# Kernel tuning notes

Hardware: AMD Instinct MI355X
Metric: run time of the kernel (lower is better)

The kernel has to match this reference:

```python
import jax, jax.numpy as jnp
import numpy as np
import math

B, S, D, H, CD = 8, 1024, 1024, 16, 512
HD = D // H
LN_EPS = 1e-5


def _layernorm(x, g, b):
    mu = jnp.mean(x, axis=-1, keepdims=True)
    var = jnp.var(x, axis=-1, keepdims=True)
    return (x - mu) / jnp.sqrt(var + LN_EPS) * g + b


def _modlin(x, code, wc_w, wc_b, ln_g, ln_b, W, b):
    # transformed_code: LayerNorm(Linear(code)) -> [D]
    tc = _layernorm(code @ wc_w.T + wc_b, ln_g, ln_b)
    return (tc * x) @ W.T + b


def setup_inputs() -> dict:
    key = jax.random.key(0)
    ks = jax.random.split(key, 16)
    inp = {
        'query': jax.random.normal(ks[0], (B, S, D), jnp.float32),
        'key': jax.random.normal(ks[1], (B, S, D), jnp.float32),
        'value': jax.random.normal(ks[2], (B, S, D), jnp.float32),
        'compability_u': jax.random.uniform(ks[3], (B, S), jnp.float32),
        'code': jax.random.normal(ks[4], (CD,), jnp.float32),
        'W': jax.random.normal(ks[5], (D, D), jnp.float32) * 0.02,
        'b': jnp.zeros((D,), jnp.float32),
    }
    for i, p in enumerate(['q', 'k', 'v', 'o']):
        inp[p + '_wc_w'] = jax.random.normal(ks[6 + i], (D, CD), jnp.float32) * 0.02
        inp[p + '_wc_b'] = jnp.zeros((D,), jnp.float32)
        inp[p + '_ln_g'] = jnp.ones((D,), jnp.float32)
        inp[p + '_ln_b'] = jnp.zeros((D,), jnp.float32)
    return inp


def reference(query, key, value, compability_u, code, W, b,
              q_wc_w, q_wc_b, q_ln_g, q_ln_b,
              k_wc_w, k_wc_b, k_ln_g, k_ln_b,
              v_wc_w, v_wc_b, v_ln_g, v_ln_b,
              o_wc_w, o_wc_b, o_ln_g, o_ln_b):
    Q = _modlin(query, code, q_wc_w, q_wc_b, q_ln_g, q_ln_b, W, b)
    K = _modlin(key, code, k_wc_w, k_wc_b, k_ln_g, k_ln_b, W, b)
    V = _modlin(value, code, v_wc_w, v_wc_b, v_ln_g, v_ln_b, W, b)
    # [B,S,D] -> [B,H,S,HD]
    Q = Q.reshape(B, S, H, HD).transpose(0, 2, 1, 3)
    K = K.reshape(B, S, H, HD).transpose(0, 2, 1, 3)
    V = V.reshape(B, S, H, HD).transpose(0, 2, 1, 3)
    energy = jnp.einsum('bhid,bhjd->bhij', Q, K) / math.sqrt(HD)
    attention = jax.nn.softmax(energy, axis=-1)
    # c_u_i[b,h,i,j] = u[b,i]; c_u_j[b,h,i,j] = u[b,j]
    attention = compability_u[:, None, :, None] * compability_u[:, None, None, :] * attention
    attention = attention / (1e-6 + attention)
    x = jnp.einsum('bhij,bhjd->bhid', attention, V)  # dropout p=0 (eval)
    x = x.transpose(0, 2, 1, 3).reshape(B, S, D)
    x = _modlin(x, code, o_wc_w, o_wc_b, o_ln_g, o_ln_b, W, b)
    return x, attention
```

## Files before the change

kernel.cpp:

```cpp
#include <hip/hip_runtime.h>
#include <hip/hip_bf16.h>
#include <stdint.h>

typedef __bf16 bf16_t;
typedef __attribute__((ext_vector_type(8))) __bf16 bf16x8;
typedef __attribute__((ext_vector_type(4))) float f32x4;

#define B_  8
#define S_  1024
#define D_  1024
#define H_  16
#define HD_ 64
#define CD_ 512

typedef __attribute__((address_space(1))) const unsigned int* gas_ptr;
typedef __attribute__((address_space(3))) unsigned int* las_ptr;

__device__ __forceinline__ void gl2lds16(const void* g, void* l) {
    __builtin_amdgcn_global_load_lds((gas_ptr)(unsigned long long)g,
                                     (las_ptr)(unsigned long long)l, 16, 0, 0);
}

__device__ __forceinline__ float clamp30(float x) {
    return fminf(fmaxf(x, -30.f), 30.f);
}

__global__ void detect_kernel(const unsigned int* Wbits, int* flag) {
    __shared__ int cnt[64];
    int c = 0;
    for (int i = threadIdx.x; i < 512; i += 64) {
        unsigned int w = Wbits[i];
        unsigned int e = (w >> 7) & 0xFFu;
        c += (e >= 0x66u && e <= 0x7Fu) ? 1 : 0;
    }
    cnt[threadIdx.x] = c;
    __syncthreads();
    if (threadIdx.x == 0) {
        int t = 0;
        for (int i = 0; i < 64; ++i) t += cnt[i];
        *flag = (t >= 280) ? 0 : 1;
    }
}

#define CANON_TOTAL 28333568u
struct CanonArgs {
    const void* src[23];
    bf16_t* dst[23];
    unsigned int off[24];
    const int* flag;
};

__global__ __launch_bounds__(256) void canon_kernel(CanonArgs a) {
    const bool f32 = (*a.flag != 0);
    const unsigned int e = ((unsigned int)blockIdx.x * 256u + threadIdx.x) * 8u;
    if (e >= CANON_TOTAL) return;
    int t = 0;
    while (e >= a.off[t + 1]) ++t;
    const unsigned int le = e - a.off[t];
    bf16_t* d = a.dst[t] + le;
    if (f32) {
        const float* s = (const float*)a.src[t] + le;
        bf16x8 o;
#pragma unroll
        for (int j = 0; j < 8; ++j) o[j] = (bf16_t)s[j];
        *(bf16x8*)d = o;
    } else {
        *(uint4*)d = *(const uint4*)((const bf16_t*)a.src[t] + le);
    }
}

struct TCArgs {
    const bf16_t* code;
    const bf16_t* bglob;
    const bf16_t* wcw[4];
    const bf16_t* wcb[4];
    const bf16_t* lng[4];
    const bf16_t* lnb[4];
    float* tc;
    float* biasArr;
};

__global__ __launch_bounds__(256) void tc_kernel(TCArgs a) {
    const int p = blockIdx.x;
    const int tid = threadIdx.x;
    __shared__ float codeS[CD_];
    __shared__ float red[256];
    __shared__ float bcast[2];
    for (int c = tid; c < CD_; c += 256) codeS[c] = (float)a.code[c];
    __syncthreads();
    float y[4];
    const bf16_t* wcw = a.wcw[p];
    for (int j = 0; j < 4; ++j) {
        const int d = tid + j * 256;
        float acc = (float)a.wcb[p][d];
        const bf16x8* row = (const bf16x8*)(wcw + (size_t)d * CD_);
        for (int c8 = 0; c8 < CD_ / 8; ++c8) {
            bf16x8 v = row[c8];
#pragma unroll
            for (int t = 0; t < 8; ++t) acc += codeS[c8 * 8 + t] * (float)v[t];
        }
        y[j] = acc;
    }
    float s = y[0] + y[1] + y[2] + y[3];
    red[tid] = s;
    __syncthreads();
    for (int off = 128; off > 0; off >>= 1) {
        if (tid < off) red[tid] += red[tid + off];
        __syncthreads();
    }
    if (tid == 0) bcast[0] = red[0] * (1.0f / (float)D_);
    __syncthreads();
    const float mu = bcast[0];
    float sq = 0.f;
    for (int j = 0; j < 4; ++j) { float t = y[j] - mu; sq += t * t; }
    red[tid] = sq;
    __syncthreads();
    for (int off = 128; off > 0; off >>= 1) {
        if (tid < off) red[tid] += red[tid + off];
        __syncthreads();
    }
    if (tid == 0) bcast[1] = red[0] * (1.0f / (float)D_);
    __syncthreads();
    const float rstd = rsqrtf(bcast[1] + 1e-5f);
    const float scale = (p == 0) ? 0.125f : 1.0f;
    for (int j = 0; j < 4; ++j) {
        const int d = tid + j * 256;
        float tcv = ((y[j] - mu) * rstd * (float)a.lng[p][d] + (float)a.lnb[p][d]) * scale;
        a.tc[p * D_ + d] = tcv;
        a.biasArr[p * D_ + d] = (float)a.bglob[d] * scale;
    }
}

__global__ __launch_bounds__(256) void wscale_kernel(const bf16_t* __restrict__ W,
                                                     const float* __restrict__ tc,
                                                     bf16_t* __restrict__ Wp) {
    const size_t idx = (size_t)blockIdx.x * 256 + threadIdx.x;
    const size_t e = idx * 8;
    const int p = (int)(e >> 20);
    const size_t rem = e & 1048575;
    const int k = (int)(rem & 1023);
    bf16x8 w = *(const bf16x8*)(W + rem);
    const float* t = tc + p * 1024 + k;
    bf16x8 o;
#pragma unroll
    for (int j = 0; j < 8; ++j) o[j] = (bf16_t)((float)w[j] * t[j]);
    *(bf16x8*)(Wp + e) = o;
}

__global__ __launch_bounds__(256) void gemm_bt(const bf16_t* __restrict__ A0,
                                               const bf16_t* __restrict__ A1,
                                               const bf16_t* __restrict__ A2,
                                               const bf16_t* __restrict__ WpAll,
                                               const float* __restrict__ biasAll,
                                               void* Cbase, int pBase, int dualOut,
                                               const int* flagp) {
    constexpr int Kd = 1024, Nd = 1024;
    __shared__ __align__(16) bf16_t As[128 * 32];
    __shared__ __align__(16) bf16_t Bs[128 * 32];
    const int tid = threadIdx.x;
    const int pl = blockIdx.y >> 6;
    const int p = pBase + pl;
    const bf16_t* A = (pl == 0) ? A0 : ((pl == 1) ? A1 : A2);
    const bf16_t* Bw = WpAll + (size_t)p * 1024 * 1024;
    const size_t cOff = (size_t)pl * 8388608;
    const int rowBase = (blockIdx.y & 63) * 128;
    const int colBase = blockIdx.x * 128;
    const int lane = tid & 63;
    const int wv = tid >> 6;
    const int wm = wv >> 1, wn = wv & 1;
    const int qd = lane >> 4, cl = lane & 15;

    f32x4 acc[4][4];
#pragma unroll
    for (int tn = 0; tn < 4; ++tn) {
        float bv = biasAll[p * 1024 + colBase + wn * 64 + tn * 16 + cl];
#pragma unroll
        for (int tm = 0; tm < 4; ++tm) acc[tm][tn] = (f32x4){bv, bv, bv, bv};
    }

    for (int kb = 0; kb < Kd; kb += 32) {
#pragma unroll
        for (int cc = 0; cc < 2; ++cc) {
            const int s = tid + cc * 256;
            const int rw = s >> 2;
            const int co = (s & 3) * 8;
            gl2lds16(A + (size_t)(rowBase + rw) * Kd + kb + co,
                     (char*)As + wv * 1024 + cc * 4096);
            gl2lds16(Bw + (size_t)(colBase + rw) * Kd + kb + co,
                     (char*)Bs + wv * 1024 + cc * 4096);
        }
        __syncthreads();
        bf16x8 aF[4], bF[4];
#pragma unroll
        for (int tm = 0; tm < 4; ++tm)
            aF[tm] = *(const bf16x8*)&As[(wm * 64 + tm * 16 + cl) * 32 + qd * 8];
#pragma unroll
        for (int tn = 0; tn < 4; ++tn)
            bF[tn] = *(const bf16x8*)&Bs[(wn * 64 + tn * 16 + cl) * 32 + qd * 8];
#pragma unroll
        for (int tm = 0; tm < 4; ++tm)
#pragma unroll
            for (int tn = 0; tn < 4; ++tn)
                acc[tm][tn] = __builtin_amdgcn_mfma_f32_16x16x32_bf16(aF[tm], bF[tn],
                                                                      acc[tm][tn], 0, 0, 0);
        __syncthreads();
    }
    const bool f32o = (dualOut != 0) && (*flagp != 0);
    if (f32o) {
        float* Cf = (float*)Cbase + cOff;
#pragma unroll
        for (int tm = 0; tm < 4; ++tm)
#pragma unroll
            for (int tn = 0; tn < 4; ++tn)
#pragma unroll
                for (int r = 0; r < 4; ++r) {
                    const int row = rowBase + wm * 64 + tm * 16 + qd * 4 + r;
                    const int col = colBase + wn * 64 + tn * 16 + cl;
                    Cf[(size_t)row * Nd + col] = acc[tm][tn][r];
                }
    } else {
        bf16_t* Cb = (bf16_t*)Cbase + cOff;
#pragma unroll
        for (int tm = 0; tm < 4; ++tm)
#pragma unroll
            for (int tn = 0; tn < 4; ++tn)
#pragma unroll
                for (int r = 0; r < 4; ++r) {
                    const int row = rowBase + wm * 64 + tm * 16 + qd * 4 + r;
                    const int col = colBase + wn * 64 + tn * 16 + cl;
                    Cb[(size_t)row * Nd + col] = (bf16_t)acc[tm][tn][r];
                }
    }
}

__global__ __launch_bounds__(256) void vtrans(const bf16_t* __restrict__ V,
                                              bf16_t* __restrict__ Vt) {
    __shared__ __align__(16) bf16_t T[64][72];
    const int bh = blockIdx.y, b = bh >> 4, h = bh & 15;
    const int s0 = blockIdx.x * 64;
    const int tid = threadIdx.x;
    const int rr = tid >> 3, cc8 = (tid & 7) * 8;
#pragma unroll
    for (int it = 0; it < 2; ++it) {
        const int sr = rr + it * 32;
        bf16x8 v = *(const bf16x8*)&V[((size_t)(b * S_ + s0 + sr)) * D_ + h * HD_ + cc8];
#pragma unroll
        for (int j = 0; j < 8; ++j) T[cc8 + j][sr] = v[j];
    }
    __syncthreads();
#pragma unroll
    for (int it = 0; it < 2; ++it) {
        const int dr = rr + it * 32;
        bf16x8 o;
#pragma unroll
        for (int j = 0; j < 8; ++j) o[j] = T[dr][cc8 + j];
        *(bf16x8*)&Vt[((size_t)bh * 64 + dr) * S_ + s0 + cc8] = o;
    }
}

__global__ __launch_bounds__(256) void attn_fused(const bf16_t* __restrict__ Q,
                                                  const bf16_t* __restrict__ Kmat,
                                                  const bf16_t* __restrict__ Vt,
                                                  const bf16_t* __restrict__ u,
                                                  void* outBase,
                                                  bf16_t* __restrict__ Xatt,
                                                  const int* flagp) {
    __shared__ __align__(16) bf16_t Ks[32 * 64];
    __shared__ __align__(16) bf16_t Vs[64 * 32];
    __shared__ __align__(16) bf16_t P[4][512];
    __shared__ __align__(16) bf16_t uS[S_];
    const int bh = blockIdx.y, b = bh >> 4, h = bh & 15;
    const int tid = threadIdx.x, lane = tid & 63, wv = tid >> 6;
    const int i0 = blockIdx.x * 64 + wv * 16;
    const int qd = lane >> 4, cl = lane & 15;
    const bool f32o = (*flagp != 0);
    float* attF = (float*)outBase + 8388608;
    bf16_t* attB = (bf16_t*)outBase + 8388608;

    for (int t = tid; t < S_ / 8; t += 256)
        *(bf16x8*)&uS[t * 8] = *(const bf16x8*)&u[b * S_ + t * 8];

    const bf16_t* Qb = Q + ((size_t)(b * S_ + i0 + cl)) * D_ + h * HD_ + qd * 8;
    bf16x8 aQ0 = *(const bf16x8*)Qb;
    bf16x8 aQ1 = *(const bf16x8*)(Qb + 32);

    const int srow_k = tid >> 3;
    const int scol_k = ((tid & 7) * 16) ^ ((srow_k & 7) << 4);
    const bf16_t* Ksrc = Kmat + ((size_t)(b * S_) + srow_k) * D_ + h * HD_ + (scol_k >> 1);
    const int srow_v = tid >> 2;
    const int scol_v = ((tid & 3) * 16) ^ ((srow_v & 3) << 4);
    const bf16_t* Vsrc = Vt + ((size_t)bh * 64 + srow_v) * S_ + (scol_v >> 1);

    f32x4 l = {0.f, 0.f, 0.f, 0.f};
    for (int jb = 0; jb < S_; jb += 32) {
        gl2lds16(Ksrc + (size_t)jb * D_, (char*)Ks + tid * 16);
        __syncthreads();
#pragma unroll
        for (int js = 0; js < 2; ++js) {
            const int rj = js * 16 + cl;
            const char* kr = (const char*)Ks + rj * 128;
            const int sw = (rj & 7) << 4;
            bf16x8 k0 = *(const bf16x8*)(kr + ((qd * 16) ^ sw));
            bf16x8 k1 = *(const bf16x8*)(kr + ((64 + qd * 16) ^ sw));
            f32x4 e = {0.f, 0.f, 0.f, 0.f};
            e = __builtin_amdgcn_mfma_f32_16x16x32_bf16(aQ0, k0, e, 0, 0, 0);
            e = __builtin_amdgcn_mfma_f32_16x16x32_bf16(aQ1, k1, e, 0, 0, 0);
            l.x += __expf(clamp30(e.x));
            l.y += __expf(clamp30(e.y));
            l.z += __expf(clamp30(e.z));
            l.w += __expf(clamp30(e.w));
        }
        __syncthreads();
    }
    for (int m = 1; m < 16; m <<= 1) {
        l.x += __shfl_xor(l.x, m);
        l.y += __shfl_xor(l.y, m);
        l.z += __shfl_xor(l.z, m);
        l.w += __shfl_xor(l.w, m);
    }
    float ui[4], el[4];
    const float lv[4] = {l.x, l.y, l.z, l.w};
#pragma unroll
    for (int r = 0; r < 4; ++r) {
        ui[r] = (float)uS[i0 + qd * 4 + r];
        el[r] = fmaxf(1e-6f * lv[r], 0.f);
    }

    f32x4 accPV[4];
#pragma unroll
    for (int dt = 0; dt < 4; ++dt) accPV[dt] = (f32x4){0.f, 0.f, 0.f, 0.f};
    bf16_t* Pw = P[wv];

    for (int jb = 0; jb < S_; jb += 32) {
        gl2lds16(Ksrc + (size_t)jb * D_, (char*)Ks + tid * 16);
        gl2lds16(Vsrc + jb, (char*)Vs + tid * 16);
        __syncthreads();
#pragma unroll
        for (int js = 0; js < 2; ++js) {
            const int rj = js * 16 + cl;
            const char* kr = (const char*)Ks + rj * 128;
            const int sw = (rj & 7) << 4;
            bf16x8 k0 = *(const bf16x8*)(kr + ((qd * 16) ^ sw));
            bf16x8 k1 = *(const bf16x8*)(kr + ((64 + qd * 16) ^ sw));
            f32x4 e = {0.f, 0.f, 0.f, 0.f};
            e = __builtin_amdgcn_mfma_f32_16x16x32_bf16(aQ0, k0, e, 0, 0, 0);
            e = __builtin_amdgcn_mfma_f32_16x16x32_bf16(aQ1, k1, e, 0, 0, 0);
            const int j0 = jb + js * 16;
            const float uj = (float)uS[j0 + cl];
#pragma unroll
            for (int r = 0; r < 4; ++r) {
                float t = __expf(clamp30(e[r]));
                float num = ui[r] * uj * t;
                float att = num * __builtin_amdgcn_rcpf(el[r] + num);
                const size_t aidx = ((size_t)bh * S_ + i0 + qd * 4 + r) * S_ + j0 + cl;
                if (f32o) attF[aidx] = att;
                else attB[aidx] = (bf16_t)att;
                Pw[(qd * 4 + r) * 32 + js * 16 + cl] = (bf16_t)att;
            }
        }
        bf16x8 pA = *(const bf16x8*)&Pw[cl * 32 + qd * 8];
#pragma unroll
        for (int dt = 0; dt < 4; ++dt) {
            const int rd = dt * 16 + cl;
            const char* vr = (const char*)Vs + rd * 64;
            bf16x8 vF = *(const bf16x8*)(vr + ((qd * 16) ^ ((rd & 3) << 4)));
            accPV[dt] = __builtin_amdgcn_mfma_f32_16x16x32_bf16(pA, vF, accPV[dt], 0, 0, 0);
        }
        __syncthreads();
    }
#pragma unroll
    for (int dt = 0; dt < 4; ++dt)
#pragma unroll
        for (int r = 0; r < 4; ++r)
            Xatt[((size_t)(b * S_ + i0 + qd * 4 + r)) * D_ + h * HD_ + dt * 16 + cl] =
                (bf16_t)accPV[dt][r];
}

extern "C" void kernel_launch(void* const* d_in, const int* in_sizes, int n_in,
                              void* d_out, int out_size, void* d_ws, size_t ws_size,
                              hipStream_t stream) {
    float* tc      = (float*)d_ws;
    float* biasArr = tc + 4096;
    bf16_t* Wp     = (bf16_t*)(biasArr + 4096);
    bf16_t* QKV    = Wp + (size_t)4 * 1048576;
    bf16_t* Xatt   = QKV + (size_t)3 * 8388608;
    bf16_t* Vt     = Xatt + 8388608;
    float* lsum    = (float*)(Vt + 8388608);
    bf16_t* smallC = (bf16_t*)(lsum + 131072);
    bf16_t* cu     = smallC;
    bf16_t* ccode  = cu + 8192;
    bf16_t* cb     = ccode + 512;
    bf16_t* cwcb   = cb + 1024;
    bf16_t* clng   = cwcb + 4096;
    bf16_t* clnb   = clng + 4096;
    int* flagp     = (int*)(clnb + 4096);

    char* canonBase = (char*)d_out + 227540992;
    bf16_t* cQ   = (bf16_t*)canonBase;
    bf16_t* cK   = cQ + 8388608;
    bf16_t* cV   = cK + 8388608;
    bf16_t* cW   = cV + 8388608;
    bf16_t* cwcw = cW + 1048576;

    detect_kernel<<<1, 64, 0, stream>>>((const unsigned int*)d_in[5], flagp);

    CanonArgs ca;
    const unsigned int offs[24] = {
        0u, 8388608u, 16777216u, 25165824u, 25174016u, 25174528u, 26223104u, 26224128u,
        26748416u, 26749440u, 26750464u, 26751488u,
        27275776u, 27276800u, 27277824u, 27278848u,
        27803136u, 27804160u, 27805184u, 27806208u,
        28330496u, 28331520u, 28332544u, 28333568u};
    for (int i = 0; i < 24; ++i) ca.off[i] = offs[i];
    ca.flag = flagp;
    ca.src[0] = d_in[0]; ca.dst[0] = cQ;
    ca.src[1] = d_in[1]; ca.dst[1] = cK;
    ca.src[2] = d_in[2]; ca.dst[2] = cV;
    ca.src[3] = d_in[3]; ca.dst[3] = cu;
    ca.src[4] = d_in[4]; ca.dst[4] = ccode;
    ca.src[5] = d_in[5]; ca.dst[5] = cW;
    ca.src[6] = d_in[6]; ca.dst[6] = cb;
    for (int p = 0; p < 4; ++p) {
        ca.src[7 + 4 * p]  = d_in[7 + 4 * p];  ca.dst[7 + 4 * p]  = cwcw + p * 524288;
        ca.src[8 + 4 * p]  = d_in[8 + 4 * p];  ca.dst[8 + 4 * p]  = cwcb + p * 1024;
        ca.src[9 + 4 * p]  = d_in[9 + 4 * p];  ca.dst[9 + 4 * p]  = clng + p * 1024;
        ca.src[10 + 4 * p] = d_in[10 + 4 * p]; ca.dst[10 + 4 * p] = clnb + p * 1024;
    }
    canon_kernel<<<13835, 256, 0, stream>>>(ca);

    TCArgs ta;
    ta.code = ccode;
    ta.bglob = cb;
    for (int p = 0; p < 4; ++p) {
        ta.wcw[p] = cwcw + p * 524288;
        ta.wcb[p] = cwcb + p * 1024;
        ta.lng[p] = clng + p * 1024;
        ta.lnb[p] = clnb + p * 1024;
    }
    ta.tc = tc;
    ta.biasArr = biasArr;
    tc_kernel<<<4, 256, 0, stream>>>(ta);

    wscale_kernel<<<2048, 256, 0, stream>>>(cW, tc, Wp);
    gemm_bt<<<dim3(8, 192), 256, 0, stream>>>(cQ, cK, cV, Wp, biasArr, QKV, 0, 0, flagp);
    vtrans<<<dim3(16, 128), 256, 0, stream>>>(QKV + (size_t)2 * 8388608, Vt);
    attn_fused<<<dim3(16, 128), 256, 0, stream>>>(QKV, QKV + 8388608, Vt, cu, d_out,
                                                  Xatt, flagp);
    gemm_bt<<<dim3(8, 64), 256, 0, stream>>>(Xatt, Xatt, Xatt, Wp, biasArr, d_out, 3, 1,
                                             flagp);
}
```

Before: 1.046 ms.

## Double-buffer K/V tiles in attention, remap block order for XCDs, raise MFMA priority

The attention kernel now double-buffers the K and V LDS tiles, prefetching the next 32-column tile while the current one is computed, and drops one barrier per iteration. Both the GEMM and attention kernels remap block IDs so that consecutive blocks on the same XCD share rows and heads, which should improve L2 reuse. s_setprio brackets around MFMA sections let compute waves take issue priority. The attention kernel uses more LDS, which may lower occupancy. The single remaining barrier per iteration must also cover the write-after-read hazard on the alternate buffer.

Result: faster. 1.006 ms (-3.8%).

```diff
diff --git a/kernel.cpp b/kernel.cpp
--- a/kernel.cpp
+++ b/kernel.cpp
@@ -158,13 +158,16 @@
     __shared__ __align__(16) bf16_t As[128 * 32];
     __shared__ __align__(16) bf16_t Bs[128 * 32];
     const int tid = threadIdx.x;
-    const int pl = blockIdx.y >> 6;
+    const int bid0 = blockIdx.x + 8 * blockIdx.y;
+    const int bids = (bid0 & 7) * gridDim.y + (bid0 >> 3);
+    const int bgx = bids & 7, bgy = bids >> 3;
+    const int pl = bgy >> 6;
     const int p = pBase + pl;
     const bf16_t* A = (pl == 0) ? A0 : ((pl == 1) ? A1 : A2);
     const bf16_t* Bw = WpAll + (size_t)p * 1024 * 1024;
     const size_t cOff = (size_t)pl * 8388608;
-    const int rowBase = (blockIdx.y & 63) * 128;
-    const int colBase = blockIdx.x * 128;
+    const int rowBase = (bgy & 63) * 128;
+    const int colBase = bgx * 128;
     const int lane = tid & 63;
     const int wv = tid >> 6;
     const int wm = wv >> 1, wn = wv & 1;
@@ -197,12 +200,14 @@
 #pragma unroll
         for (int tn = 0; tn < 4; ++tn)
             bF[tn] = *(const bf16x8*)&Bs[(wn * 64 + tn * 16 + cl) * 32 + qd * 8];
+        __builtin_amdgcn_s_setprio(1);
 #pragma unroll
         for (int tm = 0; tm < 4; ++tm)
 #pragma unroll
             for (int tn = 0; tn < 4; ++tn)
                 acc[tm][tn] = __builtin_amdgcn_mfma_f32_16x16x32_bf16(aF[tm], bF[tn],
                                                                       acc[tm][tn], 0, 0, 0);
+        __builtin_amdgcn_s_setprio(0);
         __syncthreads();
     }
     const bool f32o = (dualOut != 0) && (*flagp != 0);
@@ -265,13 +270,16 @@
                                                   void* outBase,
                                                   bf16_t* __restrict__ Xatt,
                                                   const int* flagp) {
-    __shared__ __align__(16) bf16_t Ks[32 * 64];
-    __shared__ __align__(16) bf16_t Vs[64 * 32];
+    __shared__ __align__(16) bf16_t Ks[2][32 * 64];
+    __shared__ __align__(16) bf16_t Vs[2][64 * 32];
     __shared__ __align__(16) bf16_t P[4][512];
     __shared__ __align__(16) bf16_t uS[S_];
-    const int bh = blockIdx.y, b = bh >> 4, h = bh & 15;
+    const int bid0 = blockIdx.x + 16 * blockIdx.y;
+    const int bids = (bid0 & 7) * 256 + (bid0 >> 3);
+    const int bx = bids & 15, bh = bids >> 4;
+    const int b = bh >> 4, h = bh & 15;
     const int tid = threadIdx.x, lane = tid & 63, wv = tid >> 6;
-    const int i0 = blockIdx.x * 64 + wv * 16;
+    const int i0 = bx * 64 + wv * 16;
     const int qd = lane >> 4, cl = lane & 15;
     const bool f32o = (*flagp != 0);
     float* attF = (float*)outBase + 8388608;
@@ -291,20 +299,25 @@
     const int scol_v = ((tid & 3) * 16) ^ ((srow_v & 3) << 4);
     const bf16_t* Vsrc = Vt + ((size_t)bh * 64 + srow_v) * S_ + (scol_v >> 1);
 
+    gl2lds16(Ksrc, (char*)Ks[0] + tid * 16);
+    __syncthreads();
     f32x4 l = {0.f, 0.f, 0.f, 0.f};
     for (int jb = 0; jb < S_; jb += 32) {
-        gl2lds16(Ksrc + (size_t)jb * D_, (char*)Ks + tid * 16);
-        __syncthreads();
+        const int cur = (jb >> 5) & 1;
+        if (jb + 32 < S_)
+            gl2lds16(Ksrc + (size_t)(jb + 32) * D_, (char*)Ks[cur ^ 1] + tid * 16);
 #pragma unroll
         for (int js = 0; js < 2; ++js) {
             const int rj = js * 16 + cl;
-            const char* kr = (const char*)Ks + rj * 128;
+            const char* kr = (const char*)Ks[cur] + rj * 128;
             const int sw = (rj & 7) << 4;
             bf16x8 k0 = *(const bf16x8*)(kr + ((qd * 16) ^ sw));
             bf16x8 k1 = *(const bf16x8*)(kr + ((64 + qd * 16) ^ sw));
             f32x4 e = {0.f, 0.f, 0.f, 0.f};
+            __builtin_amdgcn_s_setprio(1);
             e = __builtin_amdgcn_mfma_f32_16x16x32_bf16(aQ0, k0, e, 0, 0, 0);
             e = __builtin_amdgcn_mfma_f32_16x16x32_bf16(aQ1, k1, e, 0, 0, 0);
+            __builtin_amdgcn_s_setprio(0);
             l.x += __expf(clamp30(e.x));
             l.y += __expf(clamp30(e.y));
             l.z += __expf(clamp30(e.z));
@@ -331,20 +344,27 @@
     for (int dt = 0; dt < 4; ++dt) accPV[dt] = (f32x4){0.f, 0.f, 0.f, 0.f};
     bf16_t* Pw = P[wv];
 
+    gl2lds16(Ksrc, (char*)Ks[0] + tid * 16);
+    gl2lds16(Vsrc, (char*)Vs[0] + tid * 16);
+    __syncthreads();
     for (int jb = 0; jb < S_; jb += 32) {
-        gl2lds16(Ksrc + (size_t)jb * D_, (char*)Ks + tid * 16);
-        gl2lds16(Vsrc + jb, (char*)Vs + tid * 16);
-        __syncthreads();
+        const int cur = (jb >> 5) & 1;
+        if (jb + 32 < S_) {
+            gl2lds16(Ksrc + (size_t)(jb + 32) * D_, (char*)Ks[cur ^ 1] + tid * 16);
+            gl2lds16(Vsrc + (jb + 32), (char*)Vs[cur ^ 1] + tid * 16);
+        }
 #pragma unroll
         for (int js = 0; js < 2; ++js) {
             const int rj = js * 16 + cl;
-            const char* kr = (const char*)Ks + rj * 128;
+            const char* kr = (const char*)Ks[cur] + rj * 128;
             const int sw = (rj & 7) << 4;
             bf16x8 k0 = *(const bf16x8*)(kr + ((qd * 16) ^ sw));
             bf16x8 k1 = *(const bf16x8*)(kr + ((64 + qd * 16) ^ sw));
             f32x4 e = {0.f, 0.f, 0.f, 0.f};
+            __builtin_amdgcn_s_setprio(1);
             e = __builtin_amdgcn_mfma_f32_16x16x32_bf16(aQ0, k0, e, 0, 0, 0);
             e = __builtin_amdgcn_mfma_f32_16x16x32_bf16(aQ1, k1, e, 0, 0, 0);
+            __builtin_amdgcn_s_setprio(0);
             const int j0 = jb + js * 16;
             const float uj = (float)uS[j0 + cl];
 #pragma unroll
@@ -359,13 +379,15 @@
             }
         }
         bf16x8 pA = *(const bf16x8*)&Pw[cl * 32 + qd * 8];
+        __builtin_amdgcn_s_setprio(1);
 #pragma unroll
         for (int dt = 0; dt < 4; ++dt) {
             const int rd = dt * 16 + cl;
-            const char* vr = (const char*)Vs + rd * 64;
+            const char* vr = (const char*)Vs[cur] + rd * 64;
             bf16x8 vF = *(const bf16x8*)(vr + ((qd * 16) ^ ((rd & 3) << 4)));
             accPV[dt] = __builtin_amdgcn_mfma_f32_16x16x32_bf16(pA, vF, accPV[dt], 0, 0, 0);
         }
+        __builtin_amdgcn_s_setprio(0);
         __syncthreads();
     }
 #pragma unroll
```
